# Optimization experiments

Measured on AMD Instinct MI355X. Metric: run time of the kernel, lower is better.

The kernel has to match this reference:

```python
import jax, jax.numpy as jnp
import numpy as np

C = 128  # in_channels

def setup_inputs() -> dict:
    key = jax.random.key(0)
    k1, k2, k3, k4 = jax.random.split(key, 4)
    b, c, h, w = 4, C, 64, 64
    feature0 = jax.random.normal(k1, (b, c, h, w), dtype=jnp.float32)
    flow = jax.random.normal(k2, (b, 2, h, w), dtype=jnp.float32)
    # Linear weights stored torch-style as [out, in]; xavier-uniform-like scale
    lim = float(np.sqrt(6.0 / (c + c)))
    Wq = jax.random.uniform(k3, (c, c), minval=-lim, maxval=lim, dtype=jnp.float32)
    Wk = jax.random.uniform(k4, (c, c), minval=-lim, maxval=lim, dtype=jnp.float32)
    bq = jnp.zeros((c,), dtype=jnp.float32)
    bk = jnp.zeros((c,), dtype=jnp.float32)
    return {"feature0": feature0, "flow": flow, "Wq": Wq, "bq": bq, "Wk": Wk, "bk": bk}

def reference(feature0, flow, Wq, bq, Wk, bk):
    b, c, h, w = feature0.shape
    n = h * w
    # [b, n, c]
    x = feature0.reshape(b, c, n).transpose(0, 2, 1)
    query = x @ Wq.T + bq                     # q_proj(feature0)
    key = query @ Wk.T + bk                   # NOTE: k_proj applied to query (as in source)
    value = flow.reshape(b, flow.shape[1], n).transpose(0, 2, 1)  # [b, n, 2]
    scores = jnp.einsum('bnc,bmc->bnm', query, key) / jnp.sqrt(jnp.float32(c))
    prob = jax.nn.softmax(scores, axis=-1)    # [b, n, n]
    out = jnp.einsum('bnm,bmv->bnv', prob, value)  # [b, n, 2]
    return out.reshape(b, h, w, value.shape[-1]).transpose(0, 3, 1, 2)
```

## Files before the change

### kernel.cpp

```cpp
#include <hip/hip_runtime.h>
#include <hip/hip_bf16.h>

constexpr int CH = 128;
constexpr int NPOS = 4096;
constexpr int NB = 4;
constexpr int SPLITS = 8;

typedef __bf16 bf16x8 __attribute__((ext_vector_type(8)));
typedef float f32x16 __attribute__((ext_vector_type(16)));

constexpr float CSC = 0.08838834764831845f * 1.4426950408889634f;


__device__ __forceinline__ void async_copy16(const void* g, void* l) {
  auto gp = (const __attribute__((address_space(1))) unsigned int*)((uintptr_t)g);
  auto lp = (__attribute__((address_space(3))) unsigned int*)((uintptr_t)l);
  __builtin_amdgcn_global_load_lds(gp, lp, 16, 0, 0);
}

__global__ __launch_bounds__(128) void fuse_w_kernel(
    const float* __restrict__ Wq, const float* __restrict__ bq,
    const float* __restrict__ Wk, const float* __restrict__ bk,
    __bf16* __restrict__ Wqb, __bf16* __restrict__ Wqkb,
    float* __restrict__ bqk) {
  __shared__ float red[CH];
  const int o = blockIdx.x;
  const int i = threadIdx.x;
  float acc = 0.f;
#pragma unroll 8
  for (int m = 0; m < CH; m++) acc += Wk[o * CH + m] * Wq[m * CH + i];
  Wqkb[o * CH + i] = (__bf16)acc;
  Wqb[o * CH + i] = (__bf16)Wq[o * CH + i];
  red[i] = Wk[o * CH + i] * bq[i];
  __syncthreads();
  if (i == 0) {
    float s = 0.f;
    for (int m = 0; m < CH; m++) s += red[m];
    bqk[o] = s + bk[o];
  }
}

__global__ __launch_bounds__(64) void proj_kernel(
    const float* __restrict__ feature0, const __bf16* __restrict__ Wqb,
    const float* __restrict__ bq, const __bf16* __restrict__ Wqkb,
    const float* __restrict__ bqk, __bf16* __restrict__ Qf,
    __bf16* __restrict__ Kf) {
  const int bid = blockIdx.x;
  const int b = (bid >> 1) & 3;
  const int u = (bid >> 3) * 2 + (bid & 1);
  const int lane = threadIdx.x;
  const int half = lane >> 5, l31 = lane & 31;
  const int pos = u * 32 + l31;

  bf16x8 A[8];
#pragma unroll
  for (int ks = 0; ks < 8; ks++) {
    float v[8];
#pragma unroll
    for (int j = 0; j < 8; j++)
      v[j] = feature0[(size_t)(b * CH + ks * 16 + half * 8 + j) * NPOS + pos];
#pragma unroll
    for (int j = 0; j < 8; j++) A[ks][j] = (__bf16)v[j];
  }

#pragma unroll
  for (int z = 0; z < 2; z++) {
    const __bf16* W = z ? Wqkb : Wqb;
    const float* bias = z ? bqk : bq;
    __bf16* Out = z ? Kf : Qf;
    const float scale = z ? 1.0f : CSC;
#pragma unroll
    for (int n = 0; n < 4; n++) {
      const int co = n * 32 + l31;
      const bf16x8* Bp = (const bf16x8*)(W + co * CH + half * 8);
      f32x16 c = {0.f, 0.f, 0.f, 0.f, 0.f, 0.f, 0.f, 0.f,
                  0.f, 0.f, 0.f, 0.f, 0.f, 0.f, 0.f, 0.f};
#pragma unroll
      for (int ks = 0; ks < 8; ks++)
        c = __builtin_amdgcn_mfma_f32_32x32x16_bf16(A[ks], Bp[ks * 2], c, 0, 0,
                                                    0);
      const float bv = bias[co];
      const int kf = n * 2 + (l31 >> 4);
      const int lanebit = (l31 >> 3) & 1;
      const int j = l31 & 7;
#pragma unroll
      for (int r = 0; r < 16; r++) {
        int roff = (r & 3) + 8 * (r >> 2) + 4 * half;
        Out[((((size_t)(b * (NPOS / 32) + u)) * 8 + kf) * 64 +
             (roff + 32 * lanebit)) * 8 + j] = (__bf16)((c[r] + bv) * scale);
      }
    }
  }
}

__global__ __launch_bounds__(256, 4) void attn_kernel(
    const __bf16* __restrict__ Qf, const __bf16* __restrict__ Kf,
    const float* __restrict__ flow, float* __restrict__ part) {
  __shared__ __bf16 Klds[4][8 * 512];
  __shared__ float flds[2 * 512];
  __shared__ float red[128 * 3];

  const int bid = blockIdx.x;
  const int b = (bid >> 1) & 3;
  const int u = (bid >> 3) * 2 + (bid & 1);
  const int split = u >> 5;
  const int qg = u & 31;

  const int tid = threadIdx.x;
  const int wave = tid >> 6, lane = tid & 63;
  const int half = lane >> 5, l31 = lane & 31;
  const int kbase = split * (NPOS / SPLITS);
  constexpr int NT = NPOS / SPLITS / 32;

  {
    const float* fl0 = flow + (size_t)(b * 2 + 0) * NPOS + kbase;
    const float* fl1 = flow + (size_t)(b * 2 + 1) * NPOS + kbase;
    for (int i = tid; i < 512; i += 256) {
      flds[i] = fl0[i];
      flds[512 + i] = fl1[i];
    }
  }

  const int qt = qg * 4 + wave;
  bf16x8 qf[8];
  {
    const bf16x8* Qp =
        (const bf16x8*)Qf + ((size_t)(b * (NPOS / 32) + qt) * 8) * 64 + lane;
#pragma unroll
    for (int kf = 0; kf < 8; kf++) qf[kf] = Qp[kf * 64];
  }

  __syncthreads();

  const __bf16* Ktb =
      Kf + ((size_t)(b * (NPOS / 32) + (kbase >> 5)) * 8) * 512;

  auto issue = [&](int t) {
    const __bf16* g = Ktb + (size_t)t * (8 * 512);
#pragma unroll
    for (int cc = 0; cc < 2; cc++) {
      int chunk = wave * 2 + cc;
      async_copy16(g + chunk * 512 + lane * 8,
                   &Klds[t & 3][chunk * 512 + lane * 8]);
    }
  };
  issue(0);
  issue(1);
  issue(2);

  float ls[16], a0[16], a1[16];
#pragma unroll
  for (int r = 0; r < 16; r++) {
    ls[r] = 0.f;
    a0[r] = 0.f;
    a1[r] = 0.f;
  }

  for (int t = 0; t < NT; t++) {
    __syncthreads();
    if (t + 3 < NT) issue(t + 3);

    const __bf16* kb = &Klds[t & 3][0];
    f32x16 c = {0.f, 0.f, 0.f, 0.f, 0.f, 0.f, 0.f, 0.f,
                0.f, 0.f, 0.f, 0.f, 0.f, 0.f, 0.f, 0.f};
#pragma unroll
    for (int kf = 0; kf < 8; kf++) {
      bf16x8 bfrag = *(const bf16x8*)(kb + kf * 512 + lane * 8);
      c = __builtin_amdgcn_mfma_f32_32x32x16_bf16(qf[kf], bfrag, c, 0, 0, 0);
    }
    const float v0 = flds[t * 32 + l31];
    const float v1 = flds[512 + t * 32 + l31];
#pragma unroll
    for (int r = 0; r < 16; r++) {
      float p = exp2f(c[r]);
      ls[r] += p;
      a0[r] = fmaf(p, v0, a0[r]);
      a1[r] = fmaf(p, v1, a1[r]);
    }
  }

#pragma unroll
  for (int r = 0; r < 16; r++) {
#pragma unroll
    for (int st = 1; st < 32; st <<= 1) {
      ls[r] += __shfl_xor(ls[r], st, 64);
      a0[r] += __shfl_xor(a0[r], st, 64);
      a1[r] += __shfl_xor(a1[r], st, 64);
    }
  }
  if (l31 == 0) {
#pragma unroll
    for (int r = 0; r < 16; r++) {
      int ql = wave * 32 + (r & 3) + 8 * (r >> 2) + 4 * half;
      red[ql * 3 + 0] = ls[r];
      red[ql * 3 + 1] = a0[r];
      red[ql * 3 + 2] = a1[r];
    }
  }
  __syncthreads();
  for (int idx = tid; idx < 128 * 3; idx += 256) {
    int plane = idx / 128, ql = idx % 128;
    part[((size_t)(plane * SPLITS + split) * NB + b) * NPOS + qg * 128 + ql] =
        red[ql * 3 + plane];
  }
}

__global__ __launch_bounds__(256) void combine_kernel(
    const float* __restrict__ part, float* __restrict__ out) {
  int t = blockIdx.x * 256 + threadIdx.x;
  int b = t >> 12, q = t & (NPOS - 1);
  float l = 0.f, x = 0.f, y = 0.f;
#pragma unroll
  for (int s = 0; s < SPLITS; s++) {
    l += part[((size_t)(0 * SPLITS + s) * NB + b) * NPOS + q];
    x += part[((size_t)(1 * SPLITS + s) * NB + b) * NPOS + q];
    y += part[((size_t)(2 * SPLITS + s) * NB + b) * NPOS + q];
  }
  float inv = 1.0f / l;
  out[(size_t)(b * 2 + 0) * NPOS + q] = x * inv;
  out[(size_t)(b * 2 + 1) * NPOS + q] = y * inv;
}

extern "C" void kernel_launch(void* const* d_in, const int* in_sizes, int n_in,
                              void* d_out, int out_size, void* d_ws,
                              size_t ws_size, hipStream_t stream) {
  const float* feature0 = (const float*)d_in[0];
  const float* flow = (const float*)d_in[1];
  const float* Wq = (const float*)d_in[2];
  const float* bq = (const float*)d_in[3];
  const float* Wk = (const float*)d_in[4];
  const float* bk = (const float*)d_in[5];
  float* out = (float*)d_out;

  char* ws = (char*)d_ws;
  __bf16* Qf = (__bf16*)ws;
  __bf16* Kf = (__bf16*)(ws + (4 << 20));
  __bf16* Wqb = (__bf16*)(ws + (8 << 20));
  __bf16* Wqkb = (__bf16*)(ws + (8 << 20) + (32 << 10));
  float* bqk = (float*)(ws + (8 << 20) + (64 << 10));
  float* part = (float*)(ws + (8 << 20) + (128 << 10));

  fuse_w_kernel<<<dim3(CH), 128, 0, stream>>>(Wq, bq, Wk, bk, Wqb, Wqkb, bqk);
  proj_kernel<<<dim3(512), 64, 0, stream>>>(feature0, Wqb, bq, Wqkb, bqk, Qf,
                                            Kf);
  attn_kernel<<<dim3(1024), 256, 0, stream>>>(Qf, Kf, flow, part);
  combine_kernel<<<dim3(NB * NPOS / 256), 256, 0, stream>>>(part, out);
}
```

Measured before the change: 118.0 us.

## Use explicit vmcnt barriers with triple-buffered K tiles, packed FMA and raw exp2

The attention loop's __syncthreads is replaced by an inline-asm barrier that waits only until at most two vector-memory ops remain in flight. Async K-tile loads can then actually overlap compute instead of being fully drained every iteration. The ring buffer shrinks from four to three LDS slots, with a prefetch distance of two. The flow accumulators become f32x2 so they can use packed FMA, and exp2f is replaced by the raw hardware exp2 builtin, which skips the library's range and denormal handling. The risk is that the hand-counted vmcnt depends on exactly how many global loads each thread has issued, so it is fragile if the compiler reorders or adds memory ops.

```diff
diff --git a/kernel.cpp b/kernel.cpp
--- a/kernel.cpp
+++ b/kernel.cpp
@@ -7,6 +7,7 @@
 constexpr int SPLITS = 8;
 
 typedef __bf16 bf16x8 __attribute__((ext_vector_type(8)));
+typedef float f32x2 __attribute__((ext_vector_type(2)));
 typedef float f32x16 __attribute__((ext_vector_type(16)));
 
 constexpr float CSC = 0.08838834764831845f * 1.4426950408889634f;
@@ -17,6 +18,9 @@
   auto lp = (__attribute__((address_space(3))) unsigned int*)((uintptr_t)l);
   __builtin_amdgcn_global_load_lds(gp, lp, 16, 0, 0);
 }
+
+#define PIPE_BARRIER(N)                                              \
+  asm volatile("s_waitcnt vmcnt(" #N ") lgkmcnt(0)\n\ts_barrier" ::: "memory")
 
 __global__ __launch_bounds__(128) void fuse_w_kernel(
     const float* __restrict__ Wq, const float* __restrict__ bq,
@@ -96,7 +100,7 @@
 __global__ __launch_bounds__(256, 4) void attn_kernel(
     const __bf16* __restrict__ Qf, const __bf16* __restrict__ Kf,
     const float* __restrict__ flow, float* __restrict__ part) {
-  __shared__ __bf16 Klds[4][8 * 512];
+  __shared__ __bf16 Klds[3][8 * 512];
   __shared__ float flds[2 * 512];
   __shared__ float red[128 * 3];
 
@@ -130,37 +134,35 @@
     for (int kf = 0; kf < 8; kf++) qf[kf] = Qp[kf * 64];
   }
 
-  __syncthreads();
-
   const __bf16* Ktb =
       Kf + ((size_t)(b * (NPOS / 32) + (kbase >> 5)) * 8) * 512;
 
-  auto issue = [&](int t) {
+  auto issue = [&](int t, int buf) {
     const __bf16* g = Ktb + (size_t)t * (8 * 512);
 #pragma unroll
     for (int cc = 0; cc < 2; cc++) {
       int chunk = wave * 2 + cc;
       async_copy16(g + chunk * 512 + lane * 8,
-                   &Klds[t & 3][chunk * 512 + lane * 8]);
+                   &Klds[buf][chunk * 512 + lane * 8]);
     }
   };
-  issue(0);
-  issue(1);
-  issue(2);
-
-  float ls[16], a0[16], a1[16];
+  issue(0, 0);
+  issue(1, 1);
+
+  float ls[16];
+  f32x2 av[16];
 #pragma unroll
   for (int r = 0; r < 16; r++) {
     ls[r] = 0.f;
-    a0[r] = 0.f;
-    a1[r] = 0.f;
-  }
-
+    av[r] = f32x2{0.f, 0.f};
+  }
+
+  int bcur = 0, bnext = 2;
   for (int t = 0; t < NT; t++) {
-    __syncthreads();
-    if (t + 3 < NT) issue(t + 3);
-
-    const __bf16* kb = &Klds[t & 3][0];
+    PIPE_BARRIER(2);
+    if (t + 2 < NT) issue(t + 2, bnext);
+
+    const __bf16* kb = &Klds[bcur][0];
     f32x16 c = {0.f, 0.f, 0.f, 0.f, 0.f, 0.f, 0.f, 0.f,
                 0.f, 0.f, 0.f, 0.f, 0.f, 0.f, 0.f, 0.f};
 #pragma unroll
@@ -168,15 +170,15 @@
       bf16x8 bfrag = *(const bf16x8*)(kb + kf * 512 + lane * 8);
       c = __builtin_amdgcn_mfma_f32_32x32x16_bf16(qf[kf], bfrag, c, 0, 0, 0);
     }
-    const float v0 = flds[t * 32 + l31];
-    const float v1 = flds[512 + t * 32 + l31];
+    const f32x2 v01 = {flds[t * 32 + l31], flds[512 + t * 32 + l31]};
 #pragma unroll
     for (int r = 0; r < 16; r++) {
-      float p = exp2f(c[r]);
+      float p = __builtin_amdgcn_exp2f(c[r]);
       ls[r] += p;
-      a0[r] = fmaf(p, v0, a0[r]);
-      a1[r] = fmaf(p, v1, a1[r]);
-    }
+      av[r] += f32x2{p, p} * v01;
+    }
+    bcur = (bcur == 2) ? 0 : bcur + 1;
+    bnext = (bnext == 2) ? 0 : bnext + 1;
   }
 
 #pragma unroll
@@ -184,8 +186,8 @@
 #pragma unroll
     for (int st = 1; st < 32; st <<= 1) {
       ls[r] += __shfl_xor(ls[r], st, 64);
-      a0[r] += __shfl_xor(a0[r], st, 64);
-      a1[r] += __shfl_xor(a1[r], st, 64);
+      av[r][0] += __shfl_xor(av[r][0], st, 64);
+      av[r][1] += __shfl_xor(av[r][1], st, 64);
     }
   }
   if (l31 == 0) {
@@ -193,8 +195,8 @@
     for (int r = 0; r < 16; r++) {
       int ql = wave * 32 + (r & 3) + 8 * (r >> 2) + 4 * half;
       red[ql * 3 + 0] = ls[r];
-      red[ql * 3 + 1] = a0[r];
-      red[ql * 3 + 2] = a1[r];
+      red[ql * 3 + 1] = av[r][0];
+      red[ql * 3 + 2] = av[r][1];
     }
   }
   __syncthreads();
```

New measurement: 114.3 us. 3.1% less time.
